# Kernel tuning notes

Measured on AMD Instinct MI355X. Metric: run time of the kernel, lower is better.

Reference implementation:

```python
import jax, jax.numpy as jnp
import numpy as np

N = 50000
E = 800000
D = 128
H = 8
DH = D // H


def setup_inputs() -> dict:
    key = jax.random.key(0)
    ks = jax.random.split(key, 8)
    x = jax.random.normal(ks[0], (N, D), dtype=jnp.float32)
    src = jax.random.randint(ks[1], (E,), 0, N, dtype=jnp.int32)
    dst = jax.random.randint(ks[2], (E,), 0, N, dtype=jnp.int32)
    s = 1.0 / np.sqrt(D)
    w_qkv = jax.random.uniform(ks[3], (3 * D, D), jnp.float32, -s, s)
    b_qkv = jax.random.uniform(ks[4], (3 * D,), jnp.float32, -s, s)
    w_out = jax.random.uniform(ks[5], (D, D), jnp.float32, -s, s)
    b_out = jax.random.uniform(ks[6], (D,), jnp.float32, -s, s)
    return {"x": x, "src": src, "dst": dst, "w_qkv": w_qkv, "b_qkv": b_qkv,
            "w_out": w_out, "b_out": b_out}


def reference(x, src, dst, w_qkv, b_qkv, w_out, b_out):
    n = x.shape[0]
    coef = 1.0 / np.sqrt(DH)
    qkv = (x @ w_qkv.T + b_qkv).reshape(n, H, 3 * DH)
    q, k, v = qkv[..., :DH], qkv[..., DH:2 * DH], qkv[..., 2 * DH:]
    # per-edge scores: dot(k[src], q[dst]) per head -> [E, H]
    scores = jnp.einsum('ehd,ehd->eh', k[src], q[dst]) * coef
    # edge softmax over edges sharing the same destination node
    smax = jax.ops.segment_max(scores, dst, num_segments=n)  # [N, H]
    smax = jnp.where(jnp.isfinite(smax), smax, 0.0)
    ex = jnp.exp(scores - smax[dst])                          # [E, H]
    denom = jax.ops.segment_sum(ex, dst, num_segments=n)      # [N, H]
    probs = ex / jnp.maximum(denom[dst], 1e-30)
    # weighted aggregation of source values -> [N, H, DH]
    agg = jax.ops.segment_sum(probs[:, :, None] * v[src], dst, num_segments=n)
    out = agg.reshape(n, D) @ w_out.T + b_out
    return out
```

## Files before the change

### kernel.cpp

```cpp
#include <hip/hip_runtime.h>
#include <math.h>

#define DD   128
#define NQKV 384
#define CAP  128

typedef __attribute__((ext_vector_type(8))) short          bf16x8;
typedef __attribute__((ext_vector_type(8))) unsigned short ushort8;
typedef __attribute__((ext_vector_type(4))) float          f32x4;

__device__ __forceinline__ unsigned short f2bf(float f) {
    unsigned u = __float_as_uint(f);
    u += 0x7fffu + ((u >> 16) & 1u);
    return (unsigned short)(u >> 16);
}
__device__ __forceinline__ float bf2f(unsigned short h) {
    return __uint_as_float(((unsigned)h) << 16);
}
__device__ __forceinline__ float bflo(unsigned u) { return __uint_as_float(u << 16); }
__device__ __forceinline__ float bfhi(unsigned u) { return __uint_as_float(u & 0xffff0000u); }

#define NWQ8 (NQKV * DD / 8)
#define NWO8 (DD * DD / 8)

__global__ void prep_kernel(const float* __restrict__ w_qkv, const float* __restrict__ w_out,
                            unsigned short* __restrict__ wq_hi, unsigned short* __restrict__ wq_lo,
                            unsigned short* __restrict__ wo_hi, unsigned short* __restrict__ wo_lo,
                            int* __restrict__ counts, int nzc4) {
    int i = blockIdx.x * blockDim.x + threadIdx.x;
    if (i < nzc4) {
        ((int4*)counts)[i] = make_int4(0, 0, 0, 0);
        return;
    }
    int j = i - nzc4;
    const float* srcp;
    unsigned short *hip_, *lop_;
    if (j < NWQ8)            { srcp = w_qkv + (size_t)j * 8;          hip_ = wq_hi + (size_t)j * 8;          lop_ = wq_lo + (size_t)j * 8; }
    else if (j < NWQ8+NWO8)  { int k = j - NWQ8; srcp = w_out + (size_t)k * 8; hip_ = wo_hi + (size_t)k * 8; lop_ = wo_lo + (size_t)k * 8; }
    else return;
    const float4* p = (const float4*)srcp;
    float4 a = p[0], b = p[1];
    float v[8] = {a.x, a.y, a.z, a.w, b.x, b.y, b.z, b.w};
    ushort8 vh, vl;
    #pragma unroll
    for (int t = 0; t < 8; ++t) {
        unsigned short h = f2bf(v[t]);
        vh[t] = h;
        vl[t] = f2bf(v[t] - bf2f(h));
    }
    *(ushort8*)hip_ = vh;
    *(ushort8*)lop_ = vl;
}

__global__ void scatter_fixed_kernel(const int* __restrict__ src, const int* __restrict__ dst,
                                     int* __restrict__ counts, int* __restrict__ lists, int E) {
    int t = blockIdx.x * blockDim.x + threadIdx.x;
    int base = t * 8;
    if (base >= E) return;
    if (base + 8 <= E) {
        int4 d0 = *(const int4*)(dst + base);
        int4 d1 = *(const int4*)(dst + base + 4);
        int4 s0 = *(const int4*)(src + base);
        int4 s1 = *(const int4*)(src + base + 4);
        int dd[8] = {d0.x, d0.y, d0.z, d0.w, d1.x, d1.y, d1.z, d1.w};
        int ss[8] = {s0.x, s0.y, s0.z, s0.w, s1.x, s1.y, s1.z, s1.w};
        int pos[8];
        #pragma unroll
        for (int i = 0; i < 8; ++i) pos[i] = atomicAdd(&counts[dd[i]], 1);
        #pragma unroll
        for (int i = 0; i < 8; ++i)
            if (pos[i] < CAP) lists[(size_t)dd[i] * CAP + pos[i]] = ss[i];
    } else {
        for (int e = base; e < E; ++e) {
            int d = dst[e];
            int pos = atomicAdd(&counts[d], 1);
            if (pos < CAP) lists[(size_t)d * CAP + pos] = src[e];
        }
    }
}

#define TM 128
#define TN 128
#define LDA 40

__global__ __launch_bounds__(256, 3) void qkv_gemm_kernel(
    const float* __restrict__ X,
    const unsigned short* __restrict__ Bh, const unsigned short* __restrict__ Bl,
    const float* __restrict__ bias, unsigned short* __restrict__ Cq,
    unsigned short* __restrict__ Ck, unsigned short* __restrict__ Cv, int M)
{
    __shared__ unsigned short As[TM * LDA];
    __shared__ unsigned short Bs_h[TN * LDA];
    __shared__ unsigned short Bs_l[TN * LDA];

    const int tid  = threadIdx.x;
    const int l    = tid & 63;
    const int wv   = tid >> 6;
    const int quad = l >> 4;
    const int l15  = l & 15;
    const int wm   = (wv & 1) * 64;
    const int wn   = (wv >> 1) * 64;
    const int n0   = blockIdx.x * TN;
    const int m0   = blockIdx.y * TM;

    f32x4 acc[4][4];
    #pragma unroll
    for (int i = 0; i < 4; ++i)
        #pragma unroll
        for (int j = 0; j < 4; ++j) acc[i][j] = (f32x4)0.f;

    #pragma unroll
    for (int kc = 0; kc < DD; kc += 32) {
        #pragma unroll
        for (int it = 0; it < 2; ++it) {
            int idx = tid + it * 256;
            int row = idx >> 2;
            int pc  = idx & 3;
            int loff = row * LDA + pc * 8;
            ushort8 va = 0;
            if (m0 + row < M) {
                const float4* xp = (const float4*)(X + (size_t)(m0 + row) * DD + kc + pc * 8);
                float4 a0 = xp[0], a1 = xp[1];
                float v[8] = {a0.x,a0.y,a0.z,a0.w,a1.x,a1.y,a1.z,a1.w};
                #pragma unroll
                for (int t = 0; t < 8; ++t) va[t] = f2bf(v[t]);
            }
            *(ushort8*)&As[loff] = va;
            size_t gb = (size_t)(n0 + row) * DD + kc + pc * 8;
            *(ushort8*)&Bs_h[loff] = *(const ushort8*)(Bh + gb);
            *(ushort8*)&Bs_l[loff] = *(const ushort8*)(Bl + gb);
        }
        __syncthreads();

        bf16x8 ah[4], bh[4], bl[4];
        #pragma unroll
        for (int mt = 0; mt < 4; ++mt)
            ah[mt] = *(const bf16x8*)&As[(wm + mt * 16 + l15) * LDA + quad * 8];
        #pragma unroll
        for (int nt = 0; nt < 4; ++nt) {
            int off = (wn + nt * 16 + l15) * LDA + quad * 8;
            bh[nt] = *(const bf16x8*)&Bs_h[off];
            bl[nt] = *(const bf16x8*)&Bs_l[off];
        }
        #pragma unroll
        for (int mt = 0; mt < 4; ++mt)
            #pragma unroll
            for (int nt = 0; nt < 4; ++nt) {
                acc[mt][nt] = __builtin_amdgcn_mfma_f32_16x16x32_bf16(ah[mt], bh[nt], acc[mt][nt], 0, 0, 0);
                acc[mt][nt] = __builtin_amdgcn_mfma_f32_16x16x32_bf16(ah[mt], bl[nt], acc[mt][nt], 0, 0, 0);
            }
        __syncthreads();
    }

    #pragma unroll
    for (int nt = 0; nt < 4; ++nt) {
        int j = n0 + wn + nt * 16 + l15;
        float bj = bias[j];
        int h = j / 48;
        int r = j - h * 48;
        int seg = (r >= 32) ? 2 : ((r >= 16) ? 1 : 0);
        int bc  = h * 16 + r - seg * 16;
        unsigned short* dstp = (seg == 0 ? Cq : (seg == 1 ? Ck : Cv));
        #pragma unroll
        for (int mt = 0; mt < 4; ++mt)
            #pragma unroll
            for (int rr = 0; rr < 4; ++rr) {
                int m = m0 + wm + mt * 16 + quad * 4 + rr;
                if (m < M) dstp[(size_t)m * DD + bc] = f2bf(acc[mt][nt][rr] + bj);
            }
    }
}

__global__ __launch_bounds__(256, 3) void out_gemm_kernel(
    const unsigned short* __restrict__ A,
    const unsigned short* __restrict__ Bh, const unsigned short* __restrict__ Bl,
    const float* __restrict__ bias, float* __restrict__ C, int M)
{
    __shared__ unsigned short As[TM * LDA];
    __shared__ unsigned short Bs_h[TN * LDA];
    __shared__ unsigned short Bs_l[TN * LDA];

    const int tid  = threadIdx.x;
    const int l    = tid & 63;
    const int wv   = tid >> 6;
    const int quad = l >> 4;
    const int l15  = l & 15;
    const int wm   = (wv & 1) * 64;
    const int wn   = (wv >> 1) * 64;
    const int m0   = blockIdx.x * TM;

    f32x4 acc[4][4];
    #pragma unroll
    for (int i = 0; i < 4; ++i)
        #pragma unroll
        for (int j = 0; j < 4; ++j) acc[i][j] = (f32x4)0.f;

    #pragma unroll
    for (int kc = 0; kc < DD; kc += 32) {
        #pragma unroll
        for (int it = 0; it < 2; ++it) {
            int idx = tid + it * 256;
            int row = idx >> 2;
            int pc  = idx & 3;
            int loff = row * LDA + pc * 8;
            ushort8 va = 0;
            if (m0 + row < M)
                va = *(const ushort8*)(A + (size_t)(m0 + row) * DD + kc + pc * 8);
            *(ushort8*)&As[loff] = va;
            size_t gb = (size_t)row * DD + kc + pc * 8;
            *(ushort8*)&Bs_h[loff] = *(const ushort8*)(Bh + gb);
            *(ushort8*)&Bs_l[loff] = *(const ushort8*)(Bl + gb);
        }
        __syncthreads();

        bf16x8 ah[4], bh[4], bl[4];
        #pragma unroll
        for (int mt = 0; mt < 4; ++mt)
            ah[mt] = *(const bf16x8*)&As[(wm + mt * 16 + l15) * LDA + quad * 8];
        #pragma unroll
        for (int nt = 0; nt < 4; ++nt) {
            int off = (wn + nt * 16 + l15) * LDA + quad * 8;
            bh[nt] = *(const bf16x8*)&Bs_h[off];
            bl[nt] = *(const bf16x8*)&Bs_l[off];
        }
        #pragma unroll
        for (int mt = 0; mt < 4; ++mt)
            #pragma unroll
            for (int nt = 0; nt < 4; ++nt) {
                acc[mt][nt] = __builtin_amdgcn_mfma_f32_16x16x32_bf16(ah[mt], bh[nt], acc[mt][nt], 0, 0, 0);
                acc[mt][nt] = __builtin_amdgcn_mfma_f32_16x16x32_bf16(ah[mt], bl[nt], acc[mt][nt], 0, 0, 0);
            }
        __syncthreads();
    }

    #pragma unroll
    for (int nt = 0; nt < 4; ++nt) {
        int j = wn + nt * 16 + l15;
        float bj = bias[j];
        #pragma unroll
        for (int mt = 0; mt < 4; ++mt)
            #pragma unroll
            for (int rr = 0; rr < 4; ++rr) {
                int m = m0 + wm + mt * 16 + quad * 4 + rr;
                if (m < M) C[(size_t)m * DD + j] = acc[mt][nt][rr] + bj;
            }
    }
}

#define ATTN_BLOCKS 2048

#define ATTN_STEP(cka, ckb, cvv, nka, nkb, nvv)                                   \
  {                                                                                \
    const int cnt  = min(8, deg - c);                                              \
    const bool more = (c + 8 < deg);                                               \
    const int nn = lists[row0 + min(c + 16 + e, deg - 1)];                         \
    if (more) {                                                                    \
      const unsigned koff = (((unsigned)nxt) << 8) + hoff;                         \
      nka = *(const uint4*)(kb8 + koff);                                           \
      nkb = *(const uint4*)(kb8 + koff + 16);                                      \
      _Pragma("unroll")                                                            \
      for (int ee = 0; ee < 8; ++ee)                                               \
        nvv[ee] = *(const unsigned*)(vb8 + ((((unsigned)__shfl(nxt, ee)) << 8) + loff4)); \
    }                                                                              \
                                           \
    float sA = bflo(cka.x) * q0.x;                                                 \
    sA = fmaf(bfhi(cka.x), q0.y, sA);                                              \
    sA = fmaf(bflo(cka.y), q0.z, sA);                                              \
    sA = fmaf(bfhi(cka.y), q0.w, sA);                                              \
    float sB = bflo(cka.z) * q1.x;                                                 \
    sB = fmaf(bfhi(cka.z), q1.y, sB);                                              \
    sB = fmaf(bflo(cka.w), q1.z, sB);                                              \
    sB = fmaf(bfhi(cka.w), q1.w, sB);                                              \
    float sC = bflo(ckb.x) * q2.x;                                                 \
    sC = fmaf(bfhi(ckb.x), q2.y, sC);                                              \
    sC = fmaf(bflo(ckb.y), q2.z, sC);                                              \
    sC = fmaf(bfhi(ckb.y), q2.w, sC);                                              \
    float sD = bflo(ckb.z) * q3.x;                                                 \
    sD = fmaf(bfhi(ckb.z), q3.y, sD);                                              \
    sD = fmaf(bflo(ckb.w), q3.z, sD);                                              \
    sD = fmaf(bfhi(ckb.w), q3.w, sD);                                              \
    const float s_ = (sA + sB) + (sC + sD);                                        \
    const float pp = __expf(s_ * 0.25f);                           \
    const float p_ = (e < cnt) ? pp : 0.f;                                         \
    l_run += p_;                                                                   \
    _Pragma("unroll")                                                              \
    for (int ee = 0; ee < 8; ++ee) {                                               \
      const float pe = __shfl(p_, lbase | ee);          \
      if ((ee & 1) == 0) {                                                         \
        acc0a = fmaf(pe, bflo(cvv[ee]), acc0a);                                    \
        acc1a = fmaf(pe, bfhi(cvv[ee]), acc1a);                                    \
      } else {                                                                     \
        acc0b = fmaf(pe, bflo(cvv[ee]), acc0b);                                    \
        acc1b = fmaf(pe, bfhi(cvv[ee]), acc1b);                                    \
      }                                                                            \
    }                                                                              \
    nxt = nn;                                                                      \
    c += 8;                                                                        \
  }

__global__ __launch_bounds__(256) void wave_attn_kernel(
    const unsigned short* __restrict__ qbf, const unsigned short* __restrict__ kbf,
    const unsigned short* __restrict__ vbf, const int* __restrict__ lists,
    const int* __restrict__ counts,
    unsigned short* __restrict__ agg, int N)
{
    const int lane   = threadIdx.x & 63;
    const int wid    = blockIdx.x * 4 + (threadIdx.x >> 6);
    const int nwaves = gridDim.x * 4;

    const int h = lane >> 3;
    const int e = lane & 7;
    const unsigned hoff  = (unsigned)h << 5;
    const unsigned loff4 = (unsigned)lane << 2;
    const int lbase = lane & 0x38;

    const char* kb8 = (const char*)kbf;
    const char* vb8 = (const char*)vbf;
    const char* qb8 = (const char*)qbf;
    char*       ab8 = (char*)agg;

    for (int n = wid; n < N; n += nwaves) {
        const int deg = min(counts[n], CAP);
        const unsigned ooff = (((unsigned)n) << 8) + loff4;
        if (deg == 0) {
            *(unsigned*)(ab8 + ooff) = 0u;
            continue;
        }

        const int row0 = n * CAP;

        const unsigned qoff = (((unsigned)n) << 8) + hoff;
        const uint4 qa = *(const uint4*)(qb8 + qoff);
        const uint4 qb = *(const uint4*)(qb8 + qoff + 16);
        const float4 q0 = make_float4(bflo(qa.x), bfhi(qa.x), bflo(qa.y), bfhi(qa.y));
        const float4 q1 = make_float4(bflo(qa.z), bfhi(qa.z), bflo(qa.w), bfhi(qa.w));
        const float4 q2 = make_float4(bflo(qb.x), bfhi(qb.x), bflo(qb.y), bfhi(qb.y));
        const float4 q3 = make_float4(bflo(qb.z), bfhi(qb.z), bflo(qb.w), bfhi(qb.w));

        const int c0s = lists[row0 + min(e, deg - 1)];
        int nxt = lists[row0 + min(8 + e, deg - 1)];

        uint4 ka0, kb0, ka1, kb1;
        unsigned vv0[8], vv1[8];
        {
            const unsigned koff = (((unsigned)c0s) << 8) + hoff;
            ka0 = *(const uint4*)(kb8 + koff);
            kb0 = *(const uint4*)(kb8 + koff + 16);
            #pragma unroll
            for (int ee = 0; ee < 8; ++ee)
                vv0[ee] = *(const unsigned*)(vb8 + ((((unsigned)__shfl(c0s, ee)) << 8) + loff4));
        }
        ka1 = ka0; kb1 = kb0;
        #pragma unroll
        for (int ee = 0; ee < 8; ++ee) vv1[ee] = 0u;

        float l_run = 0.f;
        float acc0a = 0.f, acc0b = 0.f, acc1a = 0.f, acc1b = 0.f;

        int c = 0;
        for (;;) {
            ATTN_STEP(ka0, kb0, vv0, ka1, kb1, vv1);
            if (c >= deg) break;
            ATTN_STEP(ka1, kb1, vv1, ka0, kb0, vv0);
            if (c >= deg) break;
        }

        l_run += __shfl_xor(l_run, 1);
        l_run += __shfl_xor(l_run, 2);
        l_run += __shfl_xor(l_run, 4);

        const float inv = 1.f / fmaxf(l_run, 1e-30f);
        const float o0 = (acc0a + acc0b) * inv, o1 = (acc1a + acc1b) * inv;
        *(unsigned*)(ab8 + ooff) = (unsigned)f2bf(o0) | ((unsigned)f2bf(o1) << 16);
    }
}

extern "C" void kernel_launch(void* const* d_in, const int* in_sizes, int n_in,
                              void* d_out, int out_size, void* d_ws, size_t ws_size,
                              hipStream_t stream) {
    const float* x     = (const float*)d_in[0];
    const int*   src   = (const int*)  d_in[1];
    const int*   dst   = (const int*)  d_in[2];
    const float* w_qkv = (const float*)d_in[3];
    const float* b_qkv = (const float*)d_in[4];
    const float* w_out = (const float*)d_in[5];
    const float* b_out = (const float*)d_in[6];
    float* out = (float*)d_out;

    const int N = in_sizes[0] / DD;
    const int E = in_sizes[1];

    typedef unsigned short u16;
    char* ws = (char*)d_ws;
    u16* qbf   = (u16*)ws;   ws += (size_t)N * DD * sizeof(u16);
    u16* kbf   = (u16*)ws;   ws += (size_t)N * DD * sizeof(u16);
    u16* vbf   = (u16*)ws;   ws += (size_t)N * DD * sizeof(u16);
    u16* aggb  = (u16*)ws;   ws += (size_t)N * DD * sizeof(u16);
    u16* wq_hi = (u16*)ws;   ws += (size_t)NQKV * DD * sizeof(u16);
    u16* wq_lo = (u16*)ws;   ws += (size_t)NQKV * DD * sizeof(u16);
    u16* wo_hi = (u16*)ws;   ws += (size_t)DD * DD * sizeof(u16);
    u16* wo_lo = (u16*)ws;   ws += (size_t)DD * DD * sizeof(u16);
    int* counts = (int*)ws;  ws += (size_t)((N + 3) / 4 * 4) * sizeof(int);
    int* lists  = (int*)ws;  ws += (size_t)N * CAP * sizeof(int);

    const int nzc4 = (N + 3) / 4;
    const int npb  = (nzc4 + NWQ8 + NWO8 + 255) / 256;
    const int nsb  = ((E + 7) / 8 + 255) / 256;
    const int MB   = (N + TM - 1) / TM;

    prep_kernel<<<npb, 256, 0, stream>>>(w_qkv, w_out, wq_hi, wq_lo, wo_hi, wo_lo,
                                         counts, nzc4);
    scatter_fixed_kernel<<<nsb, 256, 0, stream>>>(src, dst, counts, lists, E);

    qkv_gemm_kernel<<<dim3(NQKV / TN, MB), 256, 0, stream>>>(
        x, wq_hi, wq_lo, b_qkv, qbf, kbf, vbf, N);

    wave_attn_kernel<<<ATTN_BLOCKS, 256, 0, stream>>>(
        qbf, kbf, vbf, lists, counts, aggb, N);

    out_gemm_kernel<<<MB, 256, 0, stream>>>(
        aggb, wo_hi, wo_lo, b_out, out, N);
}
```

Measured before the change: 240.3 us.

## Store Q/K/V head-major and process eight nodes per wave per head

The QKV GEMM epilogue now writes Q, K and V head-major ([H][N][16]), so one head's data for all nodes is contiguous. The attention kernel assigns each block a single head, and each wave handles eight destination nodes of that head at once, using the maximum degree across the eight as the loop bound with per-lane masking. The goal is smaller, more cache-friendly gathers per head and better lane use, at the cost of idle work when node degrees differ. Launch bounds and the attention grid size also change. N is assumed to be divisible by 8, since ngroups = N>>3 and any leftover nodes would be skipped.

After: 350.9 us. 1.46x slower.

```diff
diff --git a/kernel.cpp b/kernel.cpp
--- a/kernel.cpp
+++ b/kernel.cpp
@@ -8,6 +8,7 @@
 typedef __attribute__((ext_vector_type(8))) short          bf16x8;
 typedef __attribute__((ext_vector_type(8))) unsigned short ushort8;
 typedef __attribute__((ext_vector_type(4))) float          f32x4;
+typedef __attribute__((ext_vector_type(4))) unsigned       u32x4;
 
 __device__ __forceinline__ unsigned short f2bf(float f) {
     unsigned u = __float_as_uint(f);
@@ -159,14 +160,15 @@
         int h = j / 48;
         int r = j - h * 48;
         int seg = (r >= 32) ? 2 : ((r >= 16) ? 1 : 0);
-        int bc  = h * 16 + r - seg * 16;
+        int dim = r - seg * 16;
         unsigned short* dstp = (seg == 0 ? Cq : (seg == 1 ? Ck : Cv));
+        const size_t hb = (size_t)h * M;
         #pragma unroll
         for (int mt = 0; mt < 4; ++mt)
             #pragma unroll
             for (int rr = 0; rr < 4; ++rr) {
                 int m = m0 + wm + mt * 16 + quad * 4 + rr;
-                if (m < M) dstp[(size_t)m * DD + bc] = f2bf(acc[mt][nt][rr] + bj);
+                if (m < M) dstp[(hb + m) * 16 + dim] = f2bf(acc[mt][nt][rr] + bj);
             }
     }
 }
@@ -247,22 +249,22 @@
     }
 }
 
-#define ATTN_BLOCKS 2048
+#define ATTN_BLOCKS 1536
 
 #define ATTN_STEP(cka, ckb, cvv, nka, nkb, nvv)                                   \
   {                                                                                \
-    const int cnt  = min(8, deg - c);                                              \
-    const bool more = (c + 8 < deg);                                               \
-    const int nn = lists[row0 + min(c + 16 + e, deg - 1)];                         \
+    const bool more = (c + 8 < maxdeg);                                            \
+    int nn = lists[row0 + min(c + 16 + e, degc - 1)];                              \
+    if (deg <= 0) nn = 0;                                                          \
     if (more) {                                                                    \
-      const unsigned koff = (((unsigned)nxt) << 8) + hoff;                         \
-      nka = *(const uint4*)(kb8 + koff);                                           \
-      nkb = *(const uint4*)(kb8 + koff + 16);                                      \
+      const unsigned koff = ((unsigned)nxt) << 5;                                  \
+      nka = *(const u32x4*)(kb8 + koff);                                           \
+      nkb = *(const u32x4*)(kb8 + koff + 16);                                      \
       _Pragma("unroll")                                                            \
       for (int ee = 0; ee < 8; ++ee)                                               \
-        nvv[ee] = *(const unsigned*)(vb8 + ((((unsigned)__shfl(nxt, ee)) << 8) + loff4)); \
+        nvv[ee] = *(const unsigned*)(vb8 + ((((unsigned)__shfl(nxt, lbase | ee)) << 5) + voff)); \
     }                                                                              \
-                                           \
+                     \
     float sA = bflo(cka.x) * q0.x;                                                 \
     sA = fmaf(bfhi(cka.x), q0.y, sA);                                              \
     sA = fmaf(bflo(cka.y), q0.z, sA);                                              \
@@ -280,8 +282,7 @@
     sD = fmaf(bflo(ckb.w), q3.z, sD);                                              \
     sD = fmaf(bfhi(ckb.w), q3.w, sD);                                              \
     const float s_ = (sA + sB) + (sC + sD);                                        \
-    const float pp = __expf(s_ * 0.25f);                           \
-    const float p_ = (e < cnt) ? pp : 0.f;                                         \
+    const float p_ = (c + e < deg) ? __expf(s_ * 0.25f) : 0.f;     \
     l_run += p_;                                                                   \
     _Pragma("unroll")                                                              \
     for (int ee = 0; ee < 8; ++ee) {                                               \
@@ -298,57 +299,61 @@
     c += 8;                                                                        \
   }
 
-__global__ __launch_bounds__(256) void wave_attn_kernel(
-    const unsigned short* __restrict__ qbf, const unsigned short* __restrict__ kbf,
-    const unsigned short* __restrict__ vbf, const int* __restrict__ lists,
+__global__ __launch_bounds__(256, 6) void wave_attn_kernel(
+    const unsigned short* __restrict__ qh, const unsigned short* __restrict__ kh,
+    const unsigned short* __restrict__ vh, const int* __restrict__ lists,
     const int* __restrict__ counts,
     unsigned short* __restrict__ agg, int N)
 {
-    const int lane   = threadIdx.x & 63;
-    const int wid    = blockIdx.x * 4 + (threadIdx.x >> 6);
-    const int nwaves = gridDim.x * 4;
-
-    const int h = lane >> 3;
-    const int e = lane & 7;
-    const unsigned hoff  = (unsigned)h << 5;
-    const unsigned loff4 = (unsigned)lane << 2;
+    const int lane = threadIdx.x & 63;
+    const int head = blockIdx.x & 7;
+    const int bid8 = blockIdx.x >> 3;
+    const int wid  = bid8 * 4 + (threadIdx.x >> 6);
+    const int nwph = (gridDim.x >> 3) * 4;
+
+    const int ns = lane >> 3;
+    const int e  = lane & 7;
     const int lbase = lane & 0x38;
-
-    const char* kb8 = (const char*)kbf;
-    const char* vb8 = (const char*)vbf;
-    const char* qb8 = (const char*)qbf;
+    const unsigned voff = (unsigned)e << 2;
+
+    const char* kb8 = (const char*)kh + (size_t)head * N * 32;
+    const char* vb8 = (const char*)vh + (size_t)head * N * 32;
+    const char* qb8 = (const char*)qh + (size_t)head * N * 32;
     char*       ab8 = (char*)agg;
 
-    for (int n = wid; n < N; n += nwaves) {
-        const int deg = min(counts[n], CAP);
-        const unsigned ooff = (((unsigned)n) << 8) + loff4;
-        if (deg == 0) {
-            *(unsigned*)(ab8 + ooff) = 0u;
-            continue;
-        }
-
-        const int row0 = n * CAP;
-
-        const unsigned qoff = (((unsigned)n) << 8) + hoff;
-        const uint4 qa = *(const uint4*)(qb8 + qoff);
-        const uint4 qb = *(const uint4*)(qb8 + qoff + 16);
+    const int ngroups = N >> 3;
+    for (int g = wid; g < ngroups; g += nwph) {
+        const int node = g * 8 + ns;
+        const int deg  = min(counts[node], CAP);
+        const int degc = max(deg, 1);
+        int maxdeg = deg;
+        maxdeg = max(maxdeg, __shfl_xor(maxdeg, 8));
+        maxdeg = max(maxdeg, __shfl_xor(maxdeg, 16));
+        maxdeg = max(maxdeg, __shfl_xor(maxdeg, 32));
+
+        const int row0 = node * CAP;
+
+        const unsigned qoff = ((unsigned)node) << 5;
+        const u32x4 qa = *(const u32x4*)(qb8 + qoff);
+        const u32x4 qb = *(const u32x4*)(qb8 + qoff + 16);
         const float4 q0 = make_float4(bflo(qa.x), bfhi(qa.x), bflo(qa.y), bfhi(qa.y));
         const float4 q1 = make_float4(bflo(qa.z), bfhi(qa.z), bflo(qa.w), bfhi(qa.w));
         const float4 q2 = make_float4(bflo(qb.x), bfhi(qb.x), bflo(qb.y), bfhi(qb.y));
         const float4 q3 = make_float4(bflo(qb.z), bfhi(qb.z), bflo(qb.w), bfhi(qb.w));
 
-        const int c0s = lists[row0 + min(e, deg - 1)];
-        int nxt = lists[row0 + min(8 + e, deg - 1)];
-
-        uint4 ka0, kb0, ka1, kb1;
+        int cur = lists[row0 + min(e, degc - 1)];
+        int nxt = lists[row0 + min(8 + e, degc - 1)];
+        if (deg <= 0) { cur = 0; nxt = 0; }
+
+        u32x4 ka0, kb0, ka1, kb1;
         unsigned vv0[8], vv1[8];
         {
-            const unsigned koff = (((unsigned)c0s) << 8) + hoff;
-            ka0 = *(const uint4*)(kb8 + koff);
-            kb0 = *(const uint4*)(kb8 + koff + 16);
+            const unsigned koff = ((unsigned)cur) << 5;
+            ka0 = *(const u32x4*)(kb8 + koff);
+            kb0 = *(const u32x4*)(kb8 + koff + 16);
             #pragma unroll
             for (int ee = 0; ee < 8; ++ee)
-                vv0[ee] = *(const unsigned*)(vb8 + ((((unsigned)__shfl(c0s, ee)) << 8) + loff4));
+                vv0[ee] = *(const unsigned*)(vb8 + ((((unsigned)__shfl(cur, lbase | ee)) << 5) + voff));
         }
         ka1 = ka0; kb1 = kb0;
         #pragma unroll
@@ -358,11 +363,10 @@
         float acc0a = 0.f, acc0b = 0.f, acc1a = 0.f, acc1b = 0.f;
 
         int c = 0;
-        for (;;) {
+        while (c < maxdeg) {
             ATTN_STEP(ka0, kb0, vv0, ka1, kb1, vv1);
-            if (c >= deg) break;
+            if (c >= maxdeg) break;
             ATTN_STEP(ka1, kb1, vv1, ka0, kb0, vv0);
-            if (c >= deg) break;
         }
 
         l_run += __shfl_xor(l_run, 1);
@@ -371,6 +375,7 @@
 
         const float inv = 1.f / fmaxf(l_run, 1e-30f);
         const float o0 = (acc0a + acc0b) * inv, o1 = (acc1a + acc1b) * inv;
+        const unsigned ooff = (((unsigned)node) << 8) + ((unsigned)head << 5) + voff;
         *(unsigned*)(ab8 + ooff) = (unsigned)f2bf(o0) | ((unsigned)f2bf(o1) << 16);
     }
 }
```
